# Kernel tuning notes

Hardware: AMD Instinct MI355X
Metric: run time of the kernel (lower is better)

## Reference

```python
import jax, jax.numpy as jnp
import numpy as np

EPS = 1e-5  # BatchNorm eps

def _gcn_norm(edge_index, edge_weight, n):
    # PyG gcn_norm with add_self_loops=True, fill_value=1.0
    loop = jnp.arange(n, dtype=edge_index.dtype)
    row = jnp.concatenate([edge_index[0], loop])
    col = jnp.concatenate([edge_index[1], loop])
    ew = jnp.concatenate([edge_weight, jnp.ones((n,), edge_weight.dtype)])
    deg = jax.ops.segment_sum(ew, col, num_segments=n)
    dis = jnp.where(deg > 0, jax.lax.rsqrt(jnp.maximum(deg, 1e-30)), 0.0)
    norm = dis[row] * ew * dis[col]
    return row, col, norm

def _gcn_conv(x, W, b, row, col, norm, n):
    h = x @ W                               # [N, out]
    msg = h[row] * norm[:, None]            # gather + edge scale
    out = jax.ops.segment_sum(msg, col, num_segments=n)
    return out + b

def _bn_eval(x, gamma, beta, mean, var):
    return (x - mean) * jax.lax.rsqrt(var + EPS) * gamma + beta

def setup_inputs() -> dict:
    key = jax.random.key(0)
    ks = jax.random.split(key, 12)
    N, E, V, H = 100000, 1600000, 256, 128
    x = jax.random.normal(ks[0], (N, V), jnp.float32)
    edge_index = jax.random.randint(ks[1], (2, E), 0, N, jnp.int64)
    edge_weight = jax.random.uniform(ks[2], (E,), jnp.float32)
    s = lambda fan: 1.0 / np.sqrt(fan)
    return {
        "x": x, "edge_index": edge_index, "edge_weight": edge_weight,
        "W1": jax.random.normal(ks[3], (V, H), jnp.float32) * s(V),
        "b1": jnp.zeros((H,), jnp.float32),
        "W2": jax.random.normal(ks[4], (H, H), jnp.float32) * s(H),
        "b2": jnp.zeros((H,), jnp.float32),
        "W3": jax.random.normal(ks[5], (H, 1), jnp.float32) * s(H),
        "b3": jnp.zeros((1,), jnp.float32),
        "Wres": jax.random.normal(ks[6], (V, H), jnp.float32) * s(V),
        "g1": jnp.ones((H,), jnp.float32), "be1": jnp.zeros((H,), jnp.float32),
        "m1": jax.random.normal(ks[7], (H,), jnp.float32) * 0.01,
        "v1": jnp.ones((H,), jnp.float32),
        "g2": jnp.ones((H,), jnp.float32), "be2": jnp.zeros((H,), jnp.float32),
        "m2": jax.random.normal(ks[8], (H,), jnp.float32) * 0.01,
        "v2": jnp.ones((H,), jnp.float32),
    }

def reference(x, edge_index, edge_weight, W1, b1, W2, b2, W3, b3, Wres,
              g1, be1, m1, v1, g2, be2, m2, v2):
    n = x.shape[0]
    row, col, norm = _gcn_norm(edge_index, edge_weight, n)
    res = x @ Wres                                   # residual branch
    h = _gcn_conv(x, W1, b1, row, col, norm, n)
    h = jax.nn.relu(_bn_eval(h, g1, be1, m1, v1))    # dropout off (eval)
    h = _gcn_conv(h, W2, b2, row, col, norm, n) + res
    h = jax.nn.relu(_bn_eval(h, g2, be2, m2, v2))
    h = _gcn_conv(h, W3, b3, row, col, norm, n)      # [N, 1]
    return jnp.squeeze(h, axis=1)
```

## Files before the change

### kernel.cpp

```cpp
#include <hip/hip_runtime.h>
#include <hip/hip_bf16.h>

#define BN_EPS 1e-5f

using short8 = __attribute__((ext_vector_type(8))) short;
using f32x4  = __attribute__((ext_vector_type(4))) float;

#define FIX_SCALE 262144.0f
#define FIX_MASK  0x01ffffffu
#define CNT_ONE   (1u << 25)

static __device__ __forceinline__ unsigned short f2bf(float f) {
  unsigned int u = __float_as_uint(f);
  unsigned int r = (u + 0x7fffu + ((u >> 16) & 1u)) >> 16;
  return (unsigned short)r;
}


static __global__ void cast_weights(const float* __restrict__ W1, const float* __restrict__ Wres,
                                    const float* __restrict__ W2,
                                    unsigned short* __restrict__ B2,
                                    unsigned short* __restrict__ BT2) {
  int i = blockIdx.x * blockDim.x + threadIdx.x;
  if (i < 256 * 256) {
    int n = i >> 8, k = i & 255;
    float v = (n < 128) ? W1[k * 128 + n] : Wres[k * 128 + (n - 128)];
    B2[(k >> 5) * 8192 + n * 32 + (k & 31)] = f2bf(v);
  } else if (i < 256 * 256 + 128 * 128) {
    int j = i - 256 * 256;
    int n = j >> 7, k = j & 127;
    BT2[j] = f2bf(W2[k * 128 + n]);
  }
}


static __global__ __launch_bounds__(256)
void fused_gemm1_hist(const float* __restrict__ A, const unsigned short* __restrict__ B2,
                      unsigned short* __restrict__ C0, unsigned short* __restrict__ C1, int M,
                      const int* __restrict__ col, const float* __restrict__ ew,
                      unsigned int* __restrict__ packed,
                      unsigned short* __restrict__ rank, int E, int gB, int N) {
  __shared__ unsigned short As[2 * 64 * 40];

  int b = blockIdx.x;
  if (b >= gB) {
    unsigned int xcc;
    asm volatile("s_getreg_b32 %0, hwreg(HW_REG_XCC_ID)" : "=s"(xcc));
    xcc &= 7u;
    unsigned int* mytab = packed + (size_t)xcc * N;
    int base = (b - gB) * (256 * 4) + threadIdx.x;
#pragma unroll
    for (int j = 0; j < 4; ++j) {
      int e = base + j * 256;
      if (e < E) {
        int c = col[e];
        unsigned int fx = (unsigned int)(ew[e] * FIX_SCALE + 0.5f);
        unsigned int old = __hip_atomic_fetch_add(&mytab[c], CNT_ONE | fx,
                                                  __ATOMIC_RELAXED,
                                                  __HIP_MEMORY_SCOPE_WORKGROUP);
        rank[e] = (unsigned short)(((old >> 25) & 0x1fffu) | (xcc << 13));
      }
    }
    return;
  }

  int t = threadIdx.x;
  int wv = t >> 6, lane = t & 63;
  int quad = lane >> 4, l15 = lane & 15;
  int m0 = b * 64;

  f32x4 acc[4][4];
#pragma unroll
  for (int i = 0; i < 4; ++i)
#pragma unroll
    for (int j = 0; j < 4; ++j) acc[i][j] = (f32x4){0.f, 0.f, 0.f, 0.f};

  int ar = t >> 2;
  int ac = (t & 3) * 8;
  bool avalid = (m0 + ar) < M;
  const float* Arow = A + (size_t)(m0 + ar) * 256 + ac;
  const unsigned short* Bfrag = B2 + (wv * 64 + l15) * 32 + quad * 8;

  float4 a0 = make_float4(0.f, 0.f, 0.f, 0.f), a1 = a0;
  if (avalid) {
    a0 = *(const float4*)(Arow + 0);
    a1 = *(const float4*)(Arow + 4);
  }
  {
    short8 av;
    av[0] = (short)f2bf(a0.x); av[1] = (short)f2bf(a0.y);
    av[2] = (short)f2bf(a0.z); av[3] = (short)f2bf(a0.w);
    av[4] = (short)f2bf(a1.x); av[5] = (short)f2bf(a1.y);
    av[6] = (short)f2bf(a1.z); av[7] = (short)f2bf(a1.w);
    *(short8*)&As[ar * 40 + ac] = av;
  }
  __syncthreads();

#pragma unroll 2
  for (int s = 0; s < 8; ++s) {
    int cur = (s & 1) ? 2560 : 0;

    short8 bf[4];
#pragma unroll
    for (int nt = 0; nt < 4; ++nt)
      bf[nt] = *(const short8*)(Bfrag + s * 8192 + nt * 512);

    if (s < 7 && avalid) {
      a0 = *(const float4*)(Arow + (s + 1) * 32);
      a1 = *(const float4*)(Arow + (s + 1) * 32 + 4);
    }

    short8 af[4];
#pragma unroll
    for (int mt = 0; mt < 4; ++mt)
      af[mt] = *(const short8*)&As[cur + (mt * 16 + l15) * 40 + quad * 8];
#pragma unroll
    for (int mt = 0; mt < 4; ++mt)
#pragma unroll
      for (int nt = 0; nt < 4; ++nt)
        acc[mt][nt] = __builtin_amdgcn_mfma_f32_16x16x32_bf16(af[mt], bf[nt], acc[mt][nt], 0, 0, 0);

    if (s < 7) {
      short8 av;
      av[0] = (short)f2bf(a0.x); av[1] = (short)f2bf(a0.y);
      av[2] = (short)f2bf(a0.z); av[3] = (short)f2bf(a0.w);
      av[4] = (short)f2bf(a1.x); av[5] = (short)f2bf(a1.y);
      av[6] = (short)f2bf(a1.z); av[7] = (short)f2bf(a1.w);
      *(short8*)&As[(cur ^ 2560) + ar * 40 + ac] = av;
    }
    __syncthreads();
  }

  int nbase = wv * 64;
#pragma unroll
  for (int mt = 0; mt < 4; ++mt) {
#pragma unroll
    for (int nt = 0; nt < 4; ++nt) {
      int n = nbase + nt * 16 + l15;
#pragma unroll
      for (int reg = 0; reg < 4; ++reg) {
        size_t m = (size_t)(m0 + mt * 16 + quad * 4 + reg);
        if (nbase < 128) C0[m * 128 + n] = f2bf(acc[mt][nt][reg]);
        else             C1[m * 128 + (n - 128)] = f2bf(acc[mt][nt][reg]);
      }
    }
  }
}


#define SCAN_B 256
#define SCAN_I 16
static __global__ void scanA(const unsigned int* __restrict__ packed,
                             float* __restrict__ dis, int* __restrict__ cnt,
                             int* __restrict__ startV, int* __restrict__ blkSum, int N) {
  __shared__ int sh[SCAN_B];
  int t = threadIdx.x;
  int vbase = blockIdx.x * (SCAN_B * SCAN_I) + t * SCAN_I;
  int v[SCAN_I];
  int tot = 0;
#pragma unroll
  for (int g = 0; g < 2; ++g) {
    int c = (vbase >> 3) + g;
    int csum = 0;
    if (c < N) {
      unsigned int usum = 0;
#pragma unroll
      for (int r = 0; r < 8; ++r) {
        unsigned int pv = packed[(size_t)r * N + c];
        int cr = (int)(pv >> 25);
        v[g * 8 + r] = cr;
        csum += cr;
        usum += (pv & FIX_MASK);
      }
      cnt[c] = csum;
      dis[c] = rsqrtf(1.0f + (float)usum * (1.0f / FIX_SCALE));
    } else {
#pragma unroll
      for (int r = 0; r < 8; ++r) v[g * 8 + r] = 0;
    }
    tot += csum;
  }
  sh[t] = tot;
  __syncthreads();
  int self = tot;
  for (int off = 1; off < SCAN_B; off <<= 1) {
    int add = (t >= off) ? sh[t - off] : 0;
    __syncthreads();
    sh[t] += add;
    __syncthreads();
  }
  int excl = sh[t] - self;
  if (t == SCAN_B - 1) blkSum[blockIdx.x] = sh[t];
  int run = excl;
#pragma unroll
  for (int j = 0; j < SCAN_I; ++j) {
    if (vbase + j < 8 * N) startV[vbase + j] = run;
    run += v[j];
  }
}

static __global__ void scanB(const int* __restrict__ blkSum, int* __restrict__ blkOff, int nb) {
  __shared__ int sh[256];
  int t = threadIdx.x;
  int v = (t < nb) ? blkSum[t] : 0;
  sh[t] = v;
  __syncthreads();
  for (int off = 1; off < 256; off <<= 1) {
    int add = (t >= off) ? sh[t - off] : 0;
    __syncthreads();
    sh[t] += add;
    __syncthreads();
  }
  if (t < nb) blkOff[t] = sh[t] - v;
}

static __global__ void scanC(int* startV, const int* __restrict__ blkOff, int NV) {
  int i = blockIdx.x * blockDim.x + threadIdx.x;
  if (i < NV) startV[i] += blkOff[i / (SCAN_B * SCAN_I)];
}

static __global__ void place_kernel(const int* __restrict__ row, const int* __restrict__ col,
                                    const float* __restrict__ ew, const float* __restrict__ dis,
                                    const int* __restrict__ startV,
                                    const unsigned short* __restrict__ rank,
                                    long long* __restrict__ edges, int E) {
  int e = blockIdx.x * blockDim.x + threadIdx.x;
  if (e < E) {
    int r = row[e], c = col[e];
    unsigned int rk = rank[e];
    int pos = startV[c * 8 + (rk >> 13)] + (int)(rk & 0x1fffu);
    float nrm = dis[r] * ew[e];
    long long v = ((long long)__float_as_int(nrm) << 32) | (unsigned int)r;
    __builtin_nontemporal_store(v, &edges[pos]);
  }
}


static __global__ __launch_bounds__(256)
void gemm2_mfma(const unsigned short* __restrict__ A, const unsigned short* __restrict__ BT,
                unsigned short* __restrict__ C) {
  __shared__ unsigned short As[128 * 40];
  __shared__ unsigned short Bs[128 * 40];
  int t = threadIdx.x;
  int wv = t >> 6, lane = t & 63;
  int quad = lane >> 4, l15 = lane & 15;
  int m0 = blockIdx.x * 128;

  f32x4 acc[4][4];
#pragma unroll
  for (int i = 0; i < 4; ++i)
#pragma unroll
    for (int j = 0; j < 4; ++j) acc[i][j] = (f32x4){0.f, 0.f, 0.f, 0.f};

  int sr = t >> 1, sc = (t & 1) * 16;

  for (int k0 = 0; k0 < 128; k0 += 32) {
    short8 a0 = *(const short8*)(A + (size_t)(m0 + sr) * 128 + k0 + sc);
    short8 a1 = *(const short8*)(A + (size_t)(m0 + sr) * 128 + k0 + sc + 8);
    *(short8*)&As[sr * 40 + sc]     = a0;
    *(short8*)&As[sr * 40 + sc + 8] = a1;
    short8 b0 = *(const short8*)(BT + (size_t)sr * 128 + k0 + sc);
    short8 b1 = *(const short8*)(BT + (size_t)sr * 128 + k0 + sc + 8);
    *(short8*)&Bs[sr * 40 + sc]     = b0;
    *(short8*)&Bs[sr * 40 + sc + 8] = b1;
    __syncthreads();

    int mb = (wv >> 1) * 64, nb = (wv & 1) * 64;
    short8 af[4], bf[4];
#pragma unroll
    for (int mt = 0; mt < 4; ++mt)
      af[mt] = *(const short8*)&As[(mb + mt * 16 + l15) * 40 + quad * 8];
#pragma unroll
    for (int nt = 0; nt < 4; ++nt)
      bf[nt] = *(const short8*)&Bs[(nb + nt * 16 + l15) * 40 + quad * 8];
#pragma unroll
    for (int mt = 0; mt < 4; ++mt)
#pragma unroll
      for (int nt = 0; nt < 4; ++nt)
        acc[mt][nt] = __builtin_amdgcn_mfma_f32_16x16x32_bf16(af[mt], bf[nt], acc[mt][nt], 0, 0, 0);
    __syncthreads();
  }

  int mb = (wv >> 1) * 64, nb = (wv & 1) * 64;
#pragma unroll
  for (int mt = 0; mt < 4; ++mt)
#pragma unroll
    for (int nt = 0; nt < 4; ++nt) {
      int n = nb + nt * 16 + l15;
#pragma unroll
      for (int reg = 0; reg < 4; ++reg) {
        size_t m = (size_t)(m0 + mb + mt * 16 + quad * 4 + reg);
        C[m * 128 + n] = f2bf(acc[mt][nt][reg]);
      }
    }
}


#define PROP_GATHER_BODY                                                        \
  int c0 = lane * 2;                                                            \
  float d = dis[w];                                                             \
  float acc0, acc1;                                                             \
  {                                                                             \
    unsigned int u = Hsrc[(size_t)w * 64 + lane];                               \
    acc0 = d * __uint_as_float(u << 16);                                        \
    acc1 = d * __uint_as_float(u & 0xffff0000u);                                \
  }                                                                             \
  int s = start8[(size_t)w * 8], n = cnt[w];                                    \
  int k = 0;                                                                    \
  while (k < n) {                                                               \
    int chunk = min(n - k, 64);                                                 \
    int idx = 0;                                                                \
    float wt = 0.f;                                                             \
    if (lane < chunk) {                                                         \
      long long ev = edges[s + k + lane];                                       \
      idx = (int)(unsigned int)(ev & 0xffffffffLL);                             \
      wt  = __int_as_float((int)(ev >> 32));                                    \
    }                                                                           \
    for (int j = 0; j < chunk; j += 8) {                                        \
      int   i0 = __shfl(idx, j + 0, 64), i1 = __shfl(idx, j + 1, 64);           \
      int   i2 = __shfl(idx, j + 2, 64), i3 = __shfl(idx, j + 3, 64);           \
      int   i4 = __shfl(idx, j + 4, 64), i5 = __shfl(idx, j + 5, 64);           \
      int   i6 = __shfl(idx, j + 6, 64), i7 = __shfl(idx, j + 7, 64);           \
      float w0 = __shfl(wt, j + 0, 64), w1 = __shfl(wt, j + 1, 64);             \
      float w2 = __shfl(wt, j + 2, 64), w3 = __shfl(wt, j + 3, 64);             \
      float w4 = __shfl(wt, j + 4, 64), w5 = __shfl(wt, j + 5, 64);             \
      float w6 = __shfl(wt, j + 6, 64), w7 = __shfl(wt, j + 7, 64);             \
      unsigned int u0 = Hsrc[(size_t)i0 * 64 + lane];                           \
      unsigned int u1 = Hsrc[(size_t)i1 * 64 + lane];                           \
      unsigned int u2 = Hsrc[(size_t)i2 * 64 + lane];                           \
      unsigned int u3 = Hsrc[(size_t)i3 * 64 + lane];                           \
      unsigned int u4 = Hsrc[(size_t)i4 * 64 + lane];                           \
      unsigned int u5 = Hsrc[(size_t)i5 * 64 + lane];                           \
      unsigned int u6 = Hsrc[(size_t)i6 * 64 + lane];                           \
      unsigned int u7 = Hsrc[(size_t)i7 * 64 + lane];                           \
      acc0 = fmaf(w0, __uint_as_float(u0 << 16), acc0);                         \
      acc1 = fmaf(w0, __uint_as_float(u0 & 0xffff0000u), acc1);                 \
      acc0 = fmaf(w1, __uint_as_float(u1 << 16), acc0);                         \
      acc1 = fmaf(w1, __uint_as_float(u1 & 0xffff0000u), acc1);                 \
      acc0 = fmaf(w2, __uint_as_float(u2 << 16), acc0);                         \
      acc1 = fmaf(w2, __uint_as_float(u2 & 0xffff0000u), acc1);                 \
      acc0 = fmaf(w3, __uint_as_float(u3 << 16), acc0);                         \
      acc1 = fmaf(w3, __uint_as_float(u3 & 0xffff0000u), acc1);                 \
      acc0 = fmaf(w4, __uint_as_float(u4 << 16), acc0);                         \
      acc1 = fmaf(w4, __uint_as_float(u4 & 0xffff0000u), acc1);                 \
      acc0 = fmaf(w5, __uint_as_float(u5 << 16), acc0);                         \
      acc1 = fmaf(w5, __uint_as_float(u5 & 0xffff0000u), acc1);                 \
      acc0 = fmaf(w6, __uint_as_float(u6 << 16), acc0);                         \
      acc1 = fmaf(w6, __uint_as_float(u6 & 0xffff0000u), acc1);                 \
      acc0 = fmaf(w7, __uint_as_float(u7 << 16), acc0);                         \
      acc1 = fmaf(w7, __uint_as_float(u7 & 0xffff0000u), acc1);                 \
    }                                                                           \
    k += chunk;                                                                 \
  }                                                                             \
  acc0 *= d;                                                                    \
  acc1 *= d;

static __global__ __launch_bounds__(256)
void prop128_bf16out(const unsigned int* __restrict__ Hsrc,
                     const int* __restrict__ start8, const int* __restrict__ cnt,
                     const long long* __restrict__ edges,
                     const float* __restrict__ dis,
                     const float* __restrict__ bvec,
                     const float* __restrict__ g, const float* __restrict__ be,
                     const float* __restrict__ mean, const float* __restrict__ var,
                     unsigned int* __restrict__ Outb, int N) {
  int w = (int)((blockIdx.x * blockDim.x + threadIdx.x) >> 6);
  int lane = threadIdx.x & 63;
  if (w >= N) return;
  PROP_GATHER_BODY
  float x0 = acc0 + bvec[c0];
  float x1 = acc1 + bvec[c0 + 1];
  float s0 = g[c0] * rsqrtf(var[c0] + BN_EPS);
  float s1 = g[c0 + 1] * rsqrtf(var[c0 + 1] + BN_EPS);
  x0 = fmaxf((x0 - mean[c0]) * s0 + be[c0], 0.f);
  x1 = fmaxf((x1 - mean[c0 + 1]) * s1 + be[c0 + 1], 0.f);
  unsigned int packed = (unsigned int)f2bf(x0) | ((unsigned int)f2bf(x1) << 16);
  Outb[(size_t)w * 64 + lane] = packed;
}

static __global__ __launch_bounds__(256)
void prop128_w3out(const unsigned int* __restrict__ Hsrc,
                   const int* __restrict__ start8, const int* __restrict__ cnt,
                   const long long* __restrict__ edges,
                   const float* __restrict__ dis,
                   const float* __restrict__ bvec,
                   const float* __restrict__ g, const float* __restrict__ be,
                   const float* __restrict__ mean, const float* __restrict__ var,
                   const unsigned int* __restrict__ resb, const float* __restrict__ W3,
                   float* __restrict__ h3, int N) {
  int w = (int)((blockIdx.x * blockDim.x + threadIdx.x) >> 6);
  int lane = threadIdx.x & 63;
  if (w >= N) return;
  PROP_GATHER_BODY
  unsigned int ru = resb[(size_t)w * 64 + lane];
  float x0 = acc0 + bvec[c0]     + __uint_as_float(ru << 16);
  float x1 = acc1 + bvec[c0 + 1] + __uint_as_float(ru & 0xffff0000u);
  float s0 = g[c0] * rsqrtf(var[c0] + BN_EPS);
  float s1 = g[c0 + 1] * rsqrtf(var[c0 + 1] + BN_EPS);
  x0 = fmaxf((x0 - mean[c0]) * s0 + be[c0], 0.f);
  x1 = fmaxf((x1 - mean[c0 + 1]) * s1 + be[c0 + 1], 0.f);
  float v = x0 * W3[c0] + x1 * W3[c0 + 1];
#pragma unroll
  for (int off = 32; off > 0; off >>= 1) v += __shfl_down(v, off, 64);
  if (lane == 0) h3[w] = v;
}


static __global__ void prop3_kernel(const float* __restrict__ h3,
                                    const int* __restrict__ start8, const int* __restrict__ cnt,
                                    const long long* __restrict__ edges,
                                    const float* __restrict__ dis, const float* __restrict__ b3,
                                    float* __restrict__ out, int N) {
  int i = blockIdx.x * blockDim.x + threadIdx.x;
  if (i >= N) return;
  float d = dis[i];
  float acc = d * h3[i];
  int s = start8[(size_t)i * 8], n = cnt[i];
  for (int k = 0; k < n; ++k) {
    long long ev = edges[s + k];
    int src = (int)(unsigned int)(ev & 0xffffffffLL);
    float wt = __int_as_float((int)(ev >> 32));
    acc = fmaf(wt, h3[src], acc);
  }
  out[i] = acc * d + b3[0];
}


extern "C" void kernel_launch(void* const* d_in, const int* in_sizes, int n_in,
                              void* d_out, int out_size, void* d_ws, size_t ws_size,
                              hipStream_t stream) {
  const float* x    = (const float*)d_in[0];
  const int*   ei   = (const int*)d_in[1];
  const float* ew   = (const float*)d_in[2];
  const float* W1   = (const float*)d_in[3];
  const float* b1   = (const float*)d_in[4];
  const float* W2   = (const float*)d_in[5];
  const float* b2   = (const float*)d_in[6];
  const float* W3   = (const float*)d_in[7];
  const float* b3   = (const float*)d_in[8];
  const float* Wres = (const float*)d_in[9];
  const float* g1   = (const float*)d_in[10];
  const float* be1  = (const float*)d_in[11];
  const float* m1   = (const float*)d_in[12];
  const float* v1   = (const float*)d_in[13];
  const float* g2   = (const float*)d_in[14];
  const float* be2  = (const float*)d_in[15];
  const float* m2   = (const float*)d_in[16];
  const float* v2   = (const float*)d_in[17];

  int Hh = in_sizes[4];
  int V  = in_sizes[3] / Hh;
  int N  = in_sizes[0] / V;
  int E  = in_sizes[2];
  const int* row = ei;
  const int* col = ei + E;

  int Mp = ((N + 127) / 128) * 128;

  char* p = (char*)d_ws;
  auto alloc = [&](size_t bytes) -> char* {
    char* r = p;
    p += (bytes + 255) & ~(size_t)255;
    return r;
  };
  unsigned int* packed = (unsigned int*)alloc((size_t)N * 8 * 4);
  float* dis    = (float*)alloc((size_t)N * 4);
  int*   cnt    = (int*)  alloc((size_t)N * 4);
  int*   startV = (int*)  alloc((size_t)N * 8 * 4);
  int*   blkSum = (int*)  alloc(256 * 4);
  int*   blkOff = (int*)  alloc(256 * 4);
  unsigned short* rank = (unsigned short*)alloc((size_t)E * 2);
  long long* edges = (long long*)alloc((size_t)E * 8);
  float* h3     = (float*)alloc((size_t)N * 4);
  unsigned short* B2  = (unsigned short*)alloc((size_t)256 * 256 * 2);
  unsigned short* BT2 = (unsigned short*)alloc((size_t)128 * 128 * 2);
  unsigned short* bufG  = (unsigned short*)alloc((size_t)Mp * 128 * 2);
  unsigned short* bufH1 = (unsigned short*)alloc((size_t)Mp * 128 * 2);
  unsigned short* bufRes = (unsigned short*)alloc((size_t)Mp * 128 * 2);
  (void)ws_size; (void)n_in; (void)out_size;

  int TB = 256;
  hipMemsetAsync(packed, 0, (size_t)N * 8 * 4, stream);
  cast_weights<<<(256 * 256 + 128 * 128 + TB - 1) / TB, TB, 0, stream>>>(W1, Wres, W2, B2, BT2);

  int gB = Mp / 64;
  int hB = (E + TB * 4 - 1) / (TB * 4);
  fused_gemm1_hist<<<gB + hB, TB, 0, stream>>>(x, B2, bufG, bufRes, N,
                                               col, ew, packed, rank, E, gB, N);

  int NV = 8 * N;
  int nb = (NV + SCAN_B * SCAN_I - 1) / (SCAN_B * SCAN_I);
  scanA<<<nb, SCAN_B, 0, stream>>>(packed, dis, cnt, startV, blkSum, N);
  scanB<<<1, 256, 0, stream>>>(blkSum, blkOff, nb);
  scanC<<<(NV + TB - 1) / TB, TB, 0, stream>>>(startV, blkOff, NV);
  place_kernel<<<(E + TB - 1) / TB, TB, 0, stream>>>(row, col, ew, dis, startV,
                                                     rank, edges, E);

  int propBlocks = (int)(((size_t)N * 64 + TB - 1) / TB);
  prop128_bf16out<<<propBlocks, TB, 0, stream>>>((const unsigned int*)bufG, startV, cnt,
                                                 edges, dis, b1, g1, be1, m1, v1,
                                                 (unsigned int*)bufH1, N);

  gemm2_mfma<<<Mp / 128, 256, 0, stream>>>(bufH1, BT2, bufG);

  prop128_w3out<<<propBlocks, TB, 0, stream>>>((const unsigned int*)bufG, startV, cnt,
                                               edges, dis, b2, g2, be2, m2, v2,
                                               (const unsigned int*)bufRes, W3, h3, N);

  prop3_kernel<<<(N + TB - 1) / TB, TB, 0, stream>>>(h3, startV, cnt, edges,
                                                     dis, b3, (float*)d_out, N);
}
```

Measured before the change: 495.2 us.

## Split fused GEMM1/histogram kernel and prefetch B fragments one stage ahead

```diff
diff --git a/kernel.cpp b/kernel.cpp
--- a/kernel.cpp
+++ b/kernel.cpp
@@ -35,39 +35,38 @@
 
 
 static __global__ __launch_bounds__(256)
-void fused_gemm1_hist(const float* __restrict__ A, const unsigned short* __restrict__ B2,
-                      unsigned short* __restrict__ C0, unsigned short* __restrict__ C1, int M,
-                      const int* __restrict__ col, const float* __restrict__ ew,
-                      unsigned int* __restrict__ packed,
-                      unsigned short* __restrict__ rank, int E, int gB, int N) {
+void hist_kernel(const int* __restrict__ col, const float* __restrict__ ew,
+                 unsigned int* __restrict__ packed,
+                 unsigned short* __restrict__ rank, int E, int N) {
+  unsigned int xcc;
+  asm volatile("s_getreg_b32 %0, hwreg(HW_REG_XCC_ID)" : "=s"(xcc));
+  xcc &= 7u;
+  unsigned int* mytab = packed + (size_t)xcc * N;
+  int base = blockIdx.x * (256 * 4) + threadIdx.x;
+#pragma unroll
+  for (int j = 0; j < 4; ++j) {
+    int e = base + j * 256;
+    if (e < E) {
+      int c = col[e];
+      unsigned int fx = (unsigned int)(ew[e] * FIX_SCALE + 0.5f);
+      unsigned int old = __hip_atomic_fetch_add(&mytab[c], CNT_ONE | fx,
+                                                __ATOMIC_RELAXED,
+                                                __HIP_MEMORY_SCOPE_WORKGROUP);
+      rank[e] = (unsigned short)(((old >> 25) & 0x1fffu) | (xcc << 13));
+    }
+  }
+}
+
+
+static __global__ __launch_bounds__(256)
+void gemm1_kernel(const float* __restrict__ A, const unsigned short* __restrict__ B2,
+                  unsigned short* __restrict__ C0, unsigned short* __restrict__ C1, int M) {
   __shared__ unsigned short As[2 * 64 * 40];
-
-  int b = blockIdx.x;
-  if (b >= gB) {
-    unsigned int xcc;
-    asm volatile("s_getreg_b32 %0, hwreg(HW_REG_XCC_ID)" : "=s"(xcc));
-    xcc &= 7u;
-    unsigned int* mytab = packed + (size_t)xcc * N;
-    int base = (b - gB) * (256 * 4) + threadIdx.x;
-#pragma unroll
-    for (int j = 0; j < 4; ++j) {
-      int e = base + j * 256;
-      if (e < E) {
-        int c = col[e];
-        unsigned int fx = (unsigned int)(ew[e] * FIX_SCALE + 0.5f);
-        unsigned int old = __hip_atomic_fetch_add(&mytab[c], CNT_ONE | fx,
-                                                  __ATOMIC_RELAXED,
-                                                  __HIP_MEMORY_SCOPE_WORKGROUP);
-        rank[e] = (unsigned short)(((old >> 25) & 0x1fffu) | (xcc << 13));
-      }
-    }
-    return;
-  }
 
   int t = threadIdx.x;
   int wv = t >> 6, lane = t & 63;
   int quad = lane >> 4, l15 = lane & 15;
-  int m0 = b * 64;
+  int m0 = blockIdx.x * 64;
 
   f32x4 acc[4][4];
 #pragma unroll
@@ -94,20 +93,25 @@
     av[6] = (short)f2bf(a1.z); av[7] = (short)f2bf(a1.w);
     *(short8*)&As[ar * 40 + ac] = av;
   }
+  short8 bc[4];
+#pragma unroll
+  for (int nt = 0; nt < 4; ++nt)
+    bc[nt] = *(const short8*)(Bfrag + nt * 512);
   __syncthreads();
 
 #pragma unroll 2
   for (int s = 0; s < 8; ++s) {
     int cur = (s & 1) ? 2560 : 0;
 
-    short8 bf[4];
-#pragma unroll
-    for (int nt = 0; nt < 4; ++nt)
-      bf[nt] = *(const short8*)(Bfrag + s * 8192 + nt * 512);
-
-    if (s < 7 && avalid) {
-      a0 = *(const float4*)(Arow + (s + 1) * 32);
-      a1 = *(const float4*)(Arow + (s + 1) * 32 + 4);
+    short8 bn[4];
+    if (s < 7) {
+#pragma unroll
+      for (int nt = 0; nt < 4; ++nt)
+        bn[nt] = *(const short8*)(Bfrag + (s + 1) * 8192 + nt * 512);
+      if (avalid) {
+        a0 = *(const float4*)(Arow + (s + 1) * 32);
+        a1 = *(const float4*)(Arow + (s + 1) * 32 + 4);
+      }
     }
 
     short8 af[4];
@@ -118,7 +122,7 @@
     for (int mt = 0; mt < 4; ++mt)
 #pragma unroll
       for (int nt = 0; nt < 4; ++nt)
-        acc[mt][nt] = __builtin_amdgcn_mfma_f32_16x16x32_bf16(af[mt], bf[nt], acc[mt][nt], 0, 0, 0);
+        acc[mt][nt] = __builtin_amdgcn_mfma_f32_16x16x32_bf16(af[mt], bc[nt], acc[mt][nt], 0, 0, 0);
 
     if (s < 7) {
       short8 av;
@@ -127,6 +131,8 @@
       av[4] = (short)f2bf(a1.x); av[5] = (short)f2bf(a1.y);
       av[6] = (short)f2bf(a1.z); av[7] = (short)f2bf(a1.w);
       *(short8*)&As[(cur ^ 2560) + ar * 40 + ac] = av;
+#pragma unroll
+      for (int nt = 0; nt < 4; ++nt) bc[nt] = bn[nt];
     }
     __syncthreads();
   }
@@ -483,10 +489,9 @@
   hipMemsetAsync(packed, 0, (size_t)N * 8 * 4, stream);
   cast_weights<<<(256 * 256 + 128 * 128 + TB - 1) / TB, TB, 0, stream>>>(W1, Wres, W2, B2, BT2);
 
-  int gB = Mp / 64;
   int hB = (E + TB * 4 - 1) / (TB * 4);
-  fused_gemm1_hist<<<gB + hB, TB, 0, stream>>>(x, B2, bufG, bufRes, N,
-                                               col, ew, packed, rank, E, gB, N);
+  hist_kernel<<<hB, TB, 0, stream>>>(col, ew, packed, rank, E, N);
+  gemm1_kernel<<<Mp / 64, TB, 0, stream>>>(x, B2, bufG, bufRes, N);
 
   int NV = 8 * N;
   int nb = (NV + SCAN_B * SCAN_I - 1) / (SCAN_B * SCAN_I);
```

Result: slower. 508.4 us (+2.7%).
